# Performance work log

Hardware: AMD Instinct MI355X
Metric: run time of the kernel (lower is better)

The kernel has to match this reference:

```python
import jax, jax.numpy as jnp
import numpy as np
from jax import lax

WINDOW_SIZE = 11
SIGMA = 1.5
MAX_VAL = 1.0
C1 = (MAX_VAL * 0.01) ** 2
C2 = (MAX_VAL * 0.03) ** 2


def _make_window(channel: int, k: int = WINDOW_SIZE, sigma: float = SIGMA) -> np.ndarray:
    x = np.arange(k, dtype=np.float64)
    g = np.exp(-((x - k // 2) ** 2) / (2.0 * sigma ** 2))
    g = (g / g.sum()).astype(np.float32)
    # rank-1 separable 3D window, built as dense [C,1,k,k,k] kernel (OIDHW, groups=C)
    w3 = g[:, None, None] * g[None, :, None] * g[None, None, :]
    return np.broadcast_to(w3, (channel, 1, k, k, k)).copy()


def _dwconv3d(x, kernel, pad):
    # depthwise 3D conv, SAME padding for odd kernel
    return lax.conv_general_dilated(
        x, kernel, window_strides=(1, 1, 1), padding=[(pad, pad)] * 3,
        dimension_numbers=("NCDHW", "OIDHW", "NCDHW"),
        feature_group_count=kernel.shape[0])


def setup_inputs() -> dict:
    key = jax.random.key(0)
    k1, k2 = jax.random.split(key)
    shape = (2, 4, 64, 160, 160)  # [B, C, D, H, W]
    img1 = jax.random.uniform(k1, shape, dtype=jnp.float32)
    img2 = jax.random.uniform(k2, shape, dtype=jnp.float32)
    return {"img1": img1, "img2": img2}


def reference(img1, img2):
    channel = img1.shape[1]
    window = jnp.asarray(_make_window(channel))
    pad = WINDOW_SIZE // 2
    # mask = ones_like(img1) in the original -> identity multiply, omitted
    mu1 = _dwconv3d(img1, window, pad)
    mu2 = _dwconv3d(img2, window, pad)
    mu1_sq = mu1 * mu1
    mu2_sq = mu2 * mu2
    mu1_mu2 = mu1 * mu2
    sigma1_sq = _dwconv3d(img1 * img1, window, pad) - mu1_sq
    sigma2_sq = _dwconv3d(img2 * img2, window, pad) - mu2_sq
    sigma12 = _dwconv3d(img1 * img2, window, pad) - mu1_mu2
    ssim_map = ((2.0 * mu1_mu2 + C1) * (2.0 * sigma12 + C2)) / (
        (mu1_sq + mu2_sq + C1) * (sigma1_sq + sigma2_sq + C2))
    ssim = jnp.mean(ssim_map, axis=(0, 2, 3, 4))  # per-channel SSIM, shape [C]
    return 1.0 - ssim
```

## Files before the change

### kernel.cpp

```cpp
#include <hip/hip_runtime.h>
#include <math.h>

typedef float v2f __attribute__((ext_vector_type(2)));

namespace {

constexpr int C_DIM = 4;
constexpr int D_DIM = 64;
constexpr int H_DIM = 160;
constexpr int W_DIM = 160;

constexpr int TH = 16;
constexpr int TW = 16;
constexpr int HALO = 5;
constexpr int EH = 26;
constexpr int EW = 26;
constexpr int XST = 27;
constexpr int MST = 17;
constexpr int NPIX = EH * EW;

constexpr int TILES_W = 10;
constexpr int TPC = 100;
constexpr int D_SPLIT = 2;
constexpr int DCH = D_DIM / D_SPLIT;
constexpr int NBLOCKS = D_SPLIT * 2 * C_DIM * TPC;

constexpr float C1f = 1e-4f;
constexpr float C2f = 9e-4f;
constexpr float INV_N = 1.0f / (2.0f * 64.0f * 160.0f * 160.0f);

struct GW { float g[11]; };

}

__global__ void finalize_kernel(const float* __restrict__ partial,
                                float* __restrict__ out) {
    const int tid = threadIdx.x;
    const int c = tid >> 6;
    const int lane = tid & 63;
    float s = 0.0f;
#pragma unroll
    for (int r = 0; r < D_SPLIT * 2; ++r) {
        const int base = (r * C_DIM + c) * TPC;
        s += partial[base + lane];
        if (lane < TPC - 64) s += partial[base + 64 + lane];
    }
#pragma unroll
    for (int off = 32; off > 0; off >>= 1) s += __shfl_down(s, off, 64);
    if (lane == 0 && c < C_DIM) out[c] = 1.0f - s * INV_N;
}

__global__ __launch_bounds__(256, 3) void ssim3d_kernel(
    const float* __restrict__ img1, const float* __restrict__ img2,
    float* __restrict__ partial, GW gwp) {

    const int bid = blockIdx.x;
    const int tile = bid % TPC;
    const int c = (bid / TPC) % C_DIM;
    const int rest = bid / (TPC * C_DIM);
    const int b = rest & 1;
    const int dh = rest >> 1;
    const int h0 = (tile / TILES_W) * TH;
    const int w0 = (tile % TILES_W) * TW;

    const int d_lo = dh * DCH;
    const int s_base = (d_lo == 0) ? 0 : ((d_lo - HALO) & ~3);
    const int s_hi = min(D_DIM - 1, d_lo + DCH - 1 + HALO);
    const bool has_tail = (d_lo + DCH == D_DIM);

    const long planeHW = (long)H_DIM * W_DIM;
    const long volbase = (long)(b * C_DIM + c) * D_DIM * planeHW;
    const long org = volbase + (long)(h0 - HALO) * W_DIM + (w0 - HALO);
    const float* __restrict__ p1 = img1 + org;
    const float* __restrict__ p2 = img2 + org;

    const bool interior = (h0 >= HALO) && (h0 + TH + HALO <= H_DIM) &&
                          (w0 >= HALO) && (w0 + TW + HALO <= W_DIM);

    __shared__ v2f    xy[2][EH][XST];
    __shared__ float4 mid[2][EH][MST];
    __shared__ float  rbuf[4];

    const int tid = threadIdx.x;

    int off_[3], loff_[3];
    unsigned okmask = 0;
#pragma unroll
    for (int k = 0; k < 3; ++k) {
        const int e = tid + k * 256;
        const int hh = e / EW;
        const int ww = e - hh * EW;
        off_[k] = hh * W_DIM + ww;
        loff_[k] = hh * XST + ww;
        const int gh = h0 - HALO + hh;
        const int gw = w0 - HALO + ww;
        if (((unsigned)gh < (unsigned)H_DIM) &&
            ((unsigned)gw < (unsigned)W_DIM))
            okmask |= 1u << k;
    }
    const bool live2 = (tid < NPIX - 512);

    auto fetch_slice = [&](int s, v2f lv[3]) {
        const long sb = (long)s * planeHW;
#pragma unroll
        for (int k = 0; k < 3; ++k) {
            lv[k] = (v2f){0.0f, 0.0f};
            const bool live = (k < 2) || live2;
            if (live && (interior || ((okmask >> k) & 1u))) {
                const long gi = sb + off_[k];
                lv[k].x = p1[gi];
                lv[k].y = p2[gi];
            }
        }
    };
    auto commit_slice = [&](int buf, const v2f lv[3]) {
        v2f* base = &xy[buf][0][0];
#pragma unroll
        for (int k = 0; k < 3; ++k) {
            const bool live = (k < 2) || live2;
            if (live) base[loff_[k]] = lv[k];
        }
    };

    const bool wactive = (tid < 208);
    const int whh = tid % 26;
    const int wg2 = (tid / 26) * 2;

    auto wconv = [&](int cur) {
        v2f a0 = {0.f,0.f}, a1 = {0.f,0.f};
        v2f q0 = {0.f,0.f}, q1 = {0.f,0.f};
#pragma unroll
        for (int t = 0; t < 12; ++t) {
            const v2f xv = xy[cur][whh][wg2 + t];
            v2f qp;
            qp.x = fmaf(xv.x, xv.x, xv.y * xv.y);
            qp.y = xv.x * xv.y;
            if (t <= 10) {
                const v2f g2 = {gwp.g[t], gwp.g[t]};
                a0 = __builtin_elementwise_fma(g2, xv, a0);
                q0 = __builtin_elementwise_fma(g2, qp, q0);
            }
            if (t >= 1) {
                const v2f g2 = {gwp.g[t-1], gwp.g[t-1]};
                a1 = __builtin_elementwise_fma(g2, xv, a1);
                q1 = __builtin_elementwise_fma(g2, qp, q1);
            }
        }
        mid[cur][whh][wg2]     = make_float4(a0.x, a0.y, q0.x, q0.y);
        mid[cur][whh][wg2 + 1] = make_float4(a1.x, a1.y, q1.x, q1.y);
    };

    const int hw = tid & 15;
    const int hy = tid >> 4;

    float accum = 0.0f;
    auto ssim_add = [&](v2f mxy, v2f mqp) {
        const float m1 = mxy.x, m2 = mxy.y;
        const float q = mqp.x, pp = mqp.y;
        const float m1s = m1 * m1;
        const float m2s = m2 * m2;
        const float m12 = m1 * m2;
        const float spp = q - m1s - m2s;
        const float s12 = pp - m12;
        const float num = (2.0f * m12 + C1f) * (2.0f * s12 + C2f);
        const float den = (m1s + m2s + C1f) * (spp + C2f);
        accum = fmaf(num, __builtin_amdgcn_rcpf(den), accum);
    };

    v2f w0xy[14], w0qp[14];
#pragma unroll
    for (int i = 0; i < 14; ++i) {
        w0xy[i] = (v2f){0.f, 0.f}; w0qp[i] = (v2f){0.f, 0.f};
    }

    {
        v2f lv[3];
        fetch_slice(s_base, lv);
        commit_slice(0, lv);
    }
    __syncthreads();

    for (int sb = s_base; sb <= s_hi; sb += 4) {
#pragma unroll
        for (int u = 0; u < 4; ++u) {
            const int s = sb + u;
            if (s > s_hi) break;
            v2f lv[3];
            const bool have_next = (s + 1 <= s_hi);
            if (have_next) fetch_slice(s + 1, lv);
            if (wactive) wconv(u & 1);
            if (have_next) commit_slice((u + 1) & 1, lv);
            __syncthreads();
            {
                v2f zx = {0.f,0.f}, zq = {0.f,0.f};
#pragma unroll
                for (int t = 0; t < 11; ++t) {
                    const float4 m = mid[u & 1][hy + t][hw];
                    const v2f ma = {m.x, m.y};
                    const v2f mb = {m.z, m.w};
                    const v2f g2 = {gwp.g[t], gwp.g[t]};
                    zx = __builtin_elementwise_fma(g2, ma, zx);
                    zq = __builtin_elementwise_fma(g2, mb, zq);
                }
                w0xy[10 + u] = zx; w0qp[10 + u] = zq;
                if (s >= d_lo + HALO) {
                    v2f mx0 = {0.f,0.f}, mq0 = {0.f,0.f};
#pragma unroll
                    for (int t = 0; t < 11; ++t) {
                        const v2f g2 = {gwp.g[t], gwp.g[t]};
                        mx0 = __builtin_elementwise_fma(g2, w0xy[u + t], mx0);
                        mq0 = __builtin_elementwise_fma(g2, w0qp[u + t], mq0);
                    }
                    ssim_add(mx0, mq0);
                }
            }
        }
        {
#pragma unroll
            for (int k = 0; k < 10; ++k) {
                w0xy[k] = w0xy[k + 4]; w0qp[k] = w0qp[k + 4];
            }
        }
    }

    if (has_tail) {
#pragma unroll
        for (int i = 10; i < 14; ++i) {
            w0xy[i] = (v2f){0.f, 0.f}; w0qp[i] = (v2f){0.f, 0.f};
        }
#pragma unroll
        for (int u2 = 0; u2 < 5; ++u2) {
            v2f mx0 = {0.f,0.f}, mq0 = {0.f,0.f};
#pragma unroll
            for (int t = 0; t < 11; ++t) {
                if (u2 + t <= 13) {
                    const v2f g2 = {gwp.g[t], gwp.g[t]};
                    mx0 = __builtin_elementwise_fma(g2, w0xy[u2 + t], mx0);
                    mq0 = __builtin_elementwise_fma(g2, w0qp[u2 + t], mq0);
                }
            }
            ssim_add(mx0, mq0);
        }
    }

#pragma unroll
    for (int off = 32; off > 0; off >>= 1) accum += __shfl_down(accum, off, 64);
    const int wave = tid >> 6;
    const int lane = tid & 63;
    if (lane == 0) rbuf[wave] = accum;
    __syncthreads();
    if (tid == 0) partial[bid] = rbuf[0] + rbuf[1] + rbuf[2] + rbuf[3];
}

extern "C" void kernel_launch(void* const* d_in, const int* in_sizes, int n_in,
                              void* d_out, int out_size, void* d_ws, size_t ws_size,
                              hipStream_t stream) {
    const float* img1 = (const float*)d_in[0];
    const float* img2 = (const float*)d_in[1];
    float* out = (float*)d_out;
    float* partial = (float*)d_ws;

    GW gw;
    {
        double gd[11];
        double ssum = 0.0;
        for (int i = 0; i < 11; ++i) {
            const double t = (double)(i - 5);
            gd[i] = exp(-(t * t) / 4.5);
            ssum += gd[i];
        }
        for (int i = 0; i < 11; ++i) gw.g[i] = (float)(gd[i] / ssum);
    }

    ssim3d_kernel<<<NBLOCKS, 256, 0, stream>>>(img1, img2, partial, gw);
    finalize_kernel<<<1, 256, 0, stream>>>(partial, out);
}
```

Measured before the change: 221.6 us.

## Drop depth split, precompute squares in LDS, use SGPR-pair packed FMA weights

Each block now sweeps the full depth instead of half of it. This removes the duplicated halo slices that the depth split loaded and convolved, but halves the block count to 800. The squared and cross products are computed once when a slice is committed to LDS as a float4, rather than inside every W-convolution tap. Gaussian weights are packed as duplicated 32-bit pairs in 64-bit SGPRs and applied with inline v_pk_fma_f32, which avoids materialising broadcast vectors. Launch bounds rise to 4 blocks per CU, but the larger LDS footprint and lower parallelism may limit occupancy and latency hiding.

```diff
diff --git a/kernel.cpp b/kernel.cpp
--- a/kernel.cpp
+++ b/kernel.cpp
@@ -1,5 +1,7 @@
 #include <hip/hip_runtime.h>
 #include <math.h>
+#include <stdint.h>
+#include <string.h>
 
 typedef float v2f __attribute__((ext_vector_type(2)));
 
@@ -15,22 +17,24 @@
 constexpr int HALO = 5;
 constexpr int EH = 26;
 constexpr int EW = 26;
-constexpr int XST = 27;
+constexpr int QST = 27;
 constexpr int MST = 17;
 constexpr int NPIX = EH * EW;
 
 constexpr int TILES_W = 10;
 constexpr int TPC = 100;
-constexpr int D_SPLIT = 2;
-constexpr int DCH = D_DIM / D_SPLIT;
-constexpr int NBLOCKS = D_SPLIT * 2 * C_DIM * TPC;
+constexpr int NBLOCKS = 2 * C_DIM * TPC;
 
 constexpr float C1f = 1e-4f;
 constexpr float C2f = 9e-4f;
 constexpr float INV_N = 1.0f / (2.0f * 64.0f * 160.0f * 160.0f);
 
-struct GW { float g[11]; };
-
+struct GW { double gd[11]; };
+
+}
+
+static __device__ __forceinline__ void pk_fma(v2f& acc, v2f x, double g) {
+    asm("v_pk_fma_f32 %0, %1, %2, %0" : "+v"(acc) : "v"(x), "s"(g));
 }
 
 __global__ void finalize_kernel(const float* __restrict__ partial,
@@ -40,8 +44,8 @@
     const int lane = tid & 63;
     float s = 0.0f;
 #pragma unroll
-    for (int r = 0; r < D_SPLIT * 2; ++r) {
-        const int base = (r * C_DIM + c) * TPC;
+    for (int b = 0; b < 2; ++b) {
+        const int base = (b * C_DIM + c) * TPC;
         s += partial[base + lane];
         if (lane < TPC - 64) s += partial[base + 64 + lane];
     }
@@ -50,23 +54,16 @@
     if (lane == 0 && c < C_DIM) out[c] = 1.0f - s * INV_N;
 }
 
-__global__ __launch_bounds__(256, 3) void ssim3d_kernel(
+__global__ __launch_bounds__(256, 4) void ssim3d_kernel(
     const float* __restrict__ img1, const float* __restrict__ img2,
     float* __restrict__ partial, GW gwp) {
 
     const int bid = blockIdx.x;
     const int tile = bid % TPC;
     const int c = (bid / TPC) % C_DIM;
-    const int rest = bid / (TPC * C_DIM);
-    const int b = rest & 1;
-    const int dh = rest >> 1;
+    const int b = bid / (TPC * C_DIM);
     const int h0 = (tile / TILES_W) * TH;
     const int w0 = (tile % TILES_W) * TW;
-
-    const int d_lo = dh * DCH;
-    const int s_base = (d_lo == 0) ? 0 : ((d_lo - HALO) & ~3);
-    const int s_hi = min(D_DIM - 1, d_lo + DCH - 1 + HALO);
-    const bool has_tail = (d_lo + DCH == D_DIM);
 
     const long planeHW = (long)H_DIM * W_DIM;
     const long volbase = (long)(b * C_DIM + c) * D_DIM * planeHW;
@@ -77,7 +74,7 @@
     const bool interior = (h0 >= HALO) && (h0 + TH + HALO <= H_DIM) &&
                           (w0 >= HALO) && (w0 + TW + HALO <= W_DIM);
 
-    __shared__ v2f    xy[2][EH][XST];
+    __shared__ float4 xyqp[2][EH][QST];
     __shared__ float4 mid[2][EH][MST];
     __shared__ float  rbuf[4];
 
@@ -91,7 +88,7 @@
         const int hh = e / EW;
         const int ww = e - hh * EW;
         off_[k] = hh * W_DIM + ww;
-        loff_[k] = hh * XST + ww;
+        loff_[k] = hh * QST + ww;
         const int gh = h0 - HALO + hh;
         const int gw = w0 - HALO + ww;
         if (((unsigned)gh < (unsigned)H_DIM) &&
@@ -114,11 +111,14 @@
         }
     };
     auto commit_slice = [&](int buf, const v2f lv[3]) {
-        v2f* base = &xy[buf][0][0];
+        float4* base = &xyqp[buf][0][0];
 #pragma unroll
         for (int k = 0; k < 3; ++k) {
             const bool live = (k < 2) || live2;
-            if (live) base[loff_[k]] = lv[k];
+            if (live) {
+                const float x = lv[k].x, y = lv[k].y;
+                base[loff_[k]] = make_float4(x, y, fmaf(x, x, y * y), x * y);
+            }
         }
     };
 
@@ -131,19 +131,16 @@
         v2f q0 = {0.f,0.f}, q1 = {0.f,0.f};
 #pragma unroll
         for (int t = 0; t < 12; ++t) {
-            const v2f xv = xy[cur][whh][wg2 + t];
-            v2f qp;
-            qp.x = fmaf(xv.x, xv.x, xv.y * xv.y);
-            qp.y = xv.x * xv.y;
+            const float4 m = xyqp[cur][whh][wg2 + t];
+            const v2f xv = {m.x, m.y};
+            const v2f qp = {m.z, m.w};
             if (t <= 10) {
-                const v2f g2 = {gwp.g[t], gwp.g[t]};
-                a0 = __builtin_elementwise_fma(g2, xv, a0);
-                q0 = __builtin_elementwise_fma(g2, qp, q0);
+                pk_fma(a0, xv, gwp.gd[t]);
+                pk_fma(q0, qp, gwp.gd[t]);
             }
             if (t >= 1) {
-                const v2f g2 = {gwp.g[t-1], gwp.g[t-1]};
-                a1 = __builtin_elementwise_fma(g2, xv, a1);
-                q1 = __builtin_elementwise_fma(g2, qp, q1);
+                pk_fma(a1, xv, gwp.gd[t-1]);
+                pk_fma(q1, qp, gwp.gd[t-1]);
             }
         }
         mid[cur][whh][wg2]     = make_float4(a0.x, a0.y, q0.x, q0.y);
@@ -175,18 +172,17 @@
 
     {
         v2f lv[3];
-        fetch_slice(s_base, lv);
+        fetch_slice(0, lv);
         commit_slice(0, lv);
     }
     __syncthreads();
 
-    for (int sb = s_base; sb <= s_hi; sb += 4) {
+    for (int sb = 0; sb < D_DIM; sb += 4) {
 #pragma unroll
         for (int u = 0; u < 4; ++u) {
             const int s = sb + u;
-            if (s > s_hi) break;
             v2f lv[3];
-            const bool have_next = (s + 1 <= s_hi);
+            const bool have_next = (s + 1 < D_DIM);
             if (have_next) fetch_slice(s + 1, lv);
             if (wactive) wconv(u & 1);
             if (have_next) commit_slice((u + 1) & 1, lv);
@@ -198,18 +194,16 @@
                     const float4 m = mid[u & 1][hy + t][hw];
                     const v2f ma = {m.x, m.y};
                     const v2f mb = {m.z, m.w};
-                    const v2f g2 = {gwp.g[t], gwp.g[t]};
-                    zx = __builtin_elementwise_fma(g2, ma, zx);
-                    zq = __builtin_elementwise_fma(g2, mb, zq);
+                    pk_fma(zx, ma, gwp.gd[t]);
+                    pk_fma(zq, mb, gwp.gd[t]);
                 }
                 w0xy[10 + u] = zx; w0qp[10 + u] = zq;
-                if (s >= d_lo + HALO) {
+                if (s >= HALO) {
                     v2f mx0 = {0.f,0.f}, mq0 = {0.f,0.f};
 #pragma unroll
                     for (int t = 0; t < 11; ++t) {
-                        const v2f g2 = {gwp.g[t], gwp.g[t]};
-                        mx0 = __builtin_elementwise_fma(g2, w0xy[u + t], mx0);
-                        mq0 = __builtin_elementwise_fma(g2, w0qp[u + t], mq0);
+                        pk_fma(mx0, w0xy[u + t], gwp.gd[t]);
+                        pk_fma(mq0, w0qp[u + t], gwp.gd[t]);
                     }
                     ssim_add(mx0, mq0);
                 }
@@ -223,7 +217,7 @@
         }
     }
 
-    if (has_tail) {
+    {
 #pragma unroll
         for (int i = 10; i < 14; ++i) {
             w0xy[i] = (v2f){0.f, 0.f}; w0qp[i] = (v2f){0.f, 0.f};
@@ -234,9 +228,8 @@
 #pragma unroll
             for (int t = 0; t < 11; ++t) {
                 if (u2 + t <= 13) {
-                    const v2f g2 = {gwp.g[t], gwp.g[t]};
-                    mx0 = __builtin_elementwise_fma(g2, w0xy[u2 + t], mx0);
-                    mq0 = __builtin_elementwise_fma(g2, w0qp[u2 + t], mq0);
+                    pk_fma(mx0, w0xy[u2 + t], gwp.gd[t]);
+                    pk_fma(mq0, w0qp[u2 + t], gwp.gd[t]);
                 }
             }
             ssim_add(mx0, mq0);
@@ -269,7 +262,13 @@
             gd[i] = exp(-(t * t) / 4.5);
             ssum += gd[i];
         }
-        for (int i = 0; i < 11; ++i) gw.g[i] = (float)(gd[i] / ssum);
+        for (int i = 0; i < 11; ++i) {
+            const float gf = (float)(gd[i] / ssum);
+            uint32_t ub;
+            memcpy(&ub, &gf, 4);
+            const uint64_t up = ((uint64_t)ub << 32) | ub;
+            memcpy(&gw.gd[i], &up, 8);
+        }
     }
 
     ssim3d_kernel<<<NBLOCKS, 256, 0, stream>>>(img1, img2, partial, gw);
```

Measured after the change: 218.7 us. Within noise of the previous version (-1.3%).
